# Kernel optimization log

Hardware: AMD Instinct MI355X
Metric: run time of the kernel (lower is better)

Reference implementation:

```python
import jax, jax.numpy as jnp
import numpy as np

B, N, M = 32, 2048, 512
NUM_HEADING_BIN, NUM_SIZE_CLUSTER = 12, 8
OUT_DIM = 3 + 2 * NUM_HEADING_BIN + 4 * NUM_SIZE_CLUSTER  # 59

SPECS = [("sf_w1",64,4),("sf_w2",64,64),("sf_w3",64,64),("sf_w4",128,64),("sf_w5",1024,128),
         ("sh_w1",512,1091),("sh_w2",256,512),("sh_w3",128,256),("sh_w4",128,128),("sh_w5",2,128),
         ("t_w1",128,3),("t_w2",256,128),("t_w3",512,256),("t_fw1",256,515),("t_fw2",128,256),("t_fw3",3,128),
         ("b_w1",128,3),("b_w2",128,128),("b_w3",256,128),("b_w4",512,256),("b_fw1",512,515),("b_fw2",256,512),("b_fw3",OUT_DIM,256)]


def _bn(x, axes):
    # training-mode batch norm, gamma=1 beta=0 (fresh-init torch BatchNorm1d)
    m = jnp.mean(x, axes, keepdims=True)
    v = jnp.var(x, axes, keepdims=True)
    return (x - m) * jax.lax.rsqrt(v + 1e-5)


def _conv(x, w, b):  # 1x1 Conv1d: x (B,C,N), w (O,C), b (O,)
    return jnp.einsum('bcn,oc->bon', x, w) + b[None, :, None]


def _fc(x, w, b):  # x (B,C), w (O,C)
    return x @ w.T + b


def setup_inputs() -> dict:
    key = jax.random.key(0)
    ks = jax.random.split(key, 2 + len(SPECS))
    inp = {}
    inp["point_cloud"] = jax.random.normal(ks[0], (B, N, 4), dtype=jnp.float32)
    cls = jax.random.randint(ks[1], (B,), 0, 3)
    inp["one_hot_vec"] = jax.nn.one_hot(cls, 3, dtype=jnp.float32)
    for i, (nm, o, c) in enumerate(SPECS):
        inp[nm] = jax.random.normal(ks[2 + i], (o, c), dtype=jnp.float32) * (1.0 / np.sqrt(c))
        inp[nm.replace('w', 'b')] = jnp.zeros((o,), jnp.float32)
    return inp


def _forward(point_cloud, one_hot_vec,
             sf_w1, sf_b1, sf_w2, sf_b2, sf_w3, sf_b3, sf_w4, sf_b4, sf_w5, sf_b5,
             sh_w1, sh_b1, sh_w2, sh_b2, sh_w3, sh_b3, sh_w4, sh_b4, sh_w5, sh_b5,
             t_w1, t_b1, t_w2, t_b2, t_w3, t_b3, t_fw1, t_fb1, t_fw2, t_fb2, t_fw3, t_fb3,
             b_w1, b_b1, b_w2, b_b2, b_w3, b_b3, b_w4, b_b4, b_fw1, b_fb1, b_fw2, b_fb2, b_fw3, b_fb3):
    relu = jax.nn.relu
    Bv, Nv = point_cloud.shape[0], point_cloud.shape[1]

    # ---- PointNetSegmentation (PointNetfeat global_feat=False + seg head) ----
    x = point_cloud.transpose(0, 2, 1)                       # (B,4,N)
    h = relu(_bn(_conv(x, sf_w1, sf_b1), (0, 2)))
    pointfeat = relu(_bn(_conv(h, sf_w2, sf_b2), (0, 2)))    # (B,64,N)
    h = relu(_bn(_conv(pointfeat, sf_w3, sf_b3), (0, 2)))
    h = relu(_bn(_conv(h, sf_w4, sf_b4), (0, 2)))
    h = _bn(_conv(h, sf_w5, sf_b5), (0, 2))                  # (B,1024,N), no relu
    g = jnp.max(h, axis=2)                                   # (B,1024)
    g = jnp.concatenate([one_hot_vec, g], axis=1)            # (B,1027)
    feat = jnp.concatenate([jnp.broadcast_to(g[:, :, None], (Bv, 1027, Nv)), pointfeat], axis=1)  # (B,1091,N)
    h = relu(_bn(_conv(feat, sh_w1, sh_b1), (0, 2)))
    h = relu(_bn(_conv(h, sh_w2, sh_b2), (0, 2)))
    h = relu(_bn(_conv(h, sh_w3, sh_b3), (0, 2)))
    h = relu(_bn(_conv(h, sh_w4, sh_b4), (0, 2)))            # dropout p=0.5 -> eval identity
    logits = _conv(h, sh_w5, sh_b5).transpose(0, 2, 1)       # (B,N,2)

    # ---- point_cloud_masking: vectorized mask-select + resample-to-512 ----
    xyz = point_cloud[:, :, :3]
    mask = logits[:, :, 0] < logits[:, :, 1]                 # (B,N) bool
    cnt = jnp.sum(mask, axis=1)                              # (B,)
    mean = jnp.sum(mask[:, :, None] * xyz, axis=1) / jnp.clip(cnt, 1)[:, None].astype(xyz.dtype)
    xyz_c = xyz - mean[:, None, :]                           # centered at mask centroid
    order = jnp.argsort(jnp.logical_not(mask), axis=1, stable=True)  # masked indices first
    u = jax.random.uniform(jax.random.key(42), (Bv, M))
    pos = jnp.minimum((u * cnt[:, None].astype(u.dtype)).astype(jnp.int32),
                      jnp.maximum(cnt[:, None] - 1, 0).astype(jnp.int32))
    idx = jnp.take_along_axis(order, pos, axis=1)            # (B,M) sample w/ replacement from masked set
    object_pc = jnp.take_along_axis(xyz_c, idx[:, :, None], axis=1)  # (B,M,3)
    object_pc = jnp.where(cnt[:, None, None] > 0, object_pc, 0.0)

    x = object_pc.transpose(0, 2, 1)                         # (B,3,M)
    h = relu(_bn(_conv(x, t_w1, t_b1), (0, 2)))
    h = relu(_bn(_conv(h, t_w2, t_b2), (0, 2)))
    h = relu(_bn(_conv(h, t_w3, t_b3), (0, 2)))
    gt = jnp.max(h, axis=2)                                  # (B,512)
    gt = jnp.concatenate([one_hot_vec, gt], axis=1)          # (B,515)
    h = relu(_bn(_fc(gt, t_fw1, t_fb1), 0))
    h = relu(_bn(_fc(h, t_fw2, t_fb2), 0))
    center_delta = _fc(h, t_fw3, t_fb3)                      # (B,3)

    stage1_center = center_delta + mean
    object_pc_new = object_pc - center_delta[:, None, :]

    # ---- PointNet3DboxEstimationNet ----
    x = object_pc_new.transpose(0, 2, 1)                     # (B,3,M)
    h = relu(_bn(_conv(x, b_w1, b_b1), (0, 2)))
    h = relu(_bn(_conv(h, b_w2, b_b2), (0, 2)))
    h = relu(_bn(_conv(h, b_w3, b_b3), (0, 2)))
    h = relu(_bn(_conv(h, b_w4, b_b4), (0, 2)))
    gb = jnp.max(h, axis=2)                                  # (B,512)
    gb = jnp.concatenate([gb, one_hot_vec], axis=1)          # (B,515)
    h = relu(_bn(_fc(gb, b_fw1, b_fb1), 0))
    h = relu(_bn(_fc(h, b_fw2, b_fb2), 0))
    box_out = _fc(h, b_fw3, b_fb3)                           # (B,59)

    center = box_out[:, :3] + stage1_center                  # final box center
    return jnp.concatenate([logits.reshape(Bv, -1), box_out, center], axis=1)  # (B, 2N+59+3)


def reference(point_cloud, one_hot_vec,
              sf_w1, sf_b1, sf_w2, sf_b2, sf_w3, sf_b3, sf_w4, sf_b4, sf_w5, sf_b5,
              sh_w1, sh_b1, sh_w2, sh_b2, sh_w3, sh_b3, sh_w4, sh_b4, sh_w5, sh_b5,
              t_w1, t_b1, t_w2, t_b2, t_w3, t_b3, t_fw1, t_fb1, t_fw2, t_fb2, t_fw3, t_fb3,
              b_w1, b_b1, b_w2, b_b2, b_w3, b_b3, b_w4, b_b4, b_fw1, b_fb1, b_fw2, b_fb2, b_fw3, b_fb3):
    return _forward(point_cloud, one_hot_vec,
                    sf_w1, sf_b1, sf_w2, sf_b2, sf_w3, sf_b3, sf_w4, sf_b4, sf_w5, sf_b5,
                    sh_w1, sh_b1, sh_w2, sh_b2, sh_w3, sh_b3, sh_w4, sh_b4, sh_w5, sh_b5,
                    t_w1, t_b1, t_w2, t_b2, t_w3, t_b3, t_fw1, t_fb1, t_fw2, t_fb2, t_fw3, t_fb3,
                    b_w1, b_b1, b_w2, b_b2, b_w3, b_b3, b_w4, b_b4, b_fw1, b_fb1, b_fw2, b_fb2, b_fw3, b_fb3)
```

## Files before the change

kernel.cpp:

```cpp
#include <hip/hip_runtime.h>
#include <cstdint>


constexpr int PP   = 65536;
constexpr int PP2  = 16384;
constexpr int OUTW = 4158;

constexpr size_t F_Y1 = 0;
constexpr size_t F_Y2 = (size_t)64 * PP;
constexpr size_t F_Y3 = (size_t)128 * PP;
constexpr size_t F_Y4 = (size_t)192 * PP;
constexpr size_t F_P5S = 0;
constexpr size_t F_P5Q = (size_t)2 * 1024 * 1024;
constexpr size_t F_P5M = (size_t)128 * PP;
static_assert(F_P5Q + 2 * 1024 * 1024 <= F_Y2, "P5 partials exceed Y1 slot");
static_assert(F_P5M + 1024 * 1024 <= (size_t)192 * PP, "P5m exceeds Y3 slot");
constexpr size_t F_S1 = (size_t)320 * PP;
constexpr size_t F_S2 = 0;
constexpr size_t F_S3 = (size_t)320 * PP;
constexpr size_t F_S4 = (size_t)448 * PP;
constexpr size_t F_T1 = 0;
constexpr size_t F_T2 = F_T1 + (size_t)128 * PP2;
constexpr size_t F_PT = F_T2 + (size_t)256 * PP2;
constexpr size_t F_B1 = F_PT + (size_t)5 * 256 * 512;
constexpr size_t F_B2 = F_B1 + (size_t)128 * PP2;
constexpr size_t F_B3 = F_B2 + (size_t)128 * PP2;
constexpr size_t F_PB = F_B3 + (size_t)256 * PP2;
static_assert(F_PB + (size_t)5 * 256 * 512 <= (size_t)256 * PP, "t/b overlay overflow");
static_assert((F_PT % 2) == 0 && (F_PB % 2) == 0, "double alignment");

constexpr size_t SB       = (size_t)832 * PP;
constexpr size_t F_MASK   = SB;
constexpr size_t F_MIDX   = F_MASK + PP;
constexpr size_t F_CNT    = F_MIDX + PP;
constexpr size_t F_MEAN   = F_CNT + 32;
constexpr size_t F_GVEC   = F_MEAN + 96;
constexpr size_t F_GVT    = F_GVEC + 32 * 1027;
constexpr size_t F_GVB    = F_GVT + 32 * 515;
constexpr size_t F_GDOT   = F_GVB + 32 * 515;
constexpr size_t F_YT1    = F_GDOT + 512 * 32;
constexpr size_t F_YT2    = F_YT1 + 32 * 256;
constexpr size_t F_YB1    = F_YT2 + 32 * 128;
constexpr size_t F_YB2    = F_YB1 + 32 * 512;
constexpr size_t F_CD     = F_YB2 + 32 * 256;
constexpr size_t F_OBJ    = F_CD + 96;
constexpr size_t F_ST     = F_OBJ + (size_t)3 * PP2;
constexpr size_t F_END    = F_ST + 20 * 2048;
constexpr size_t NEED_BYTES = F_END * 4;

#define NEG_INF (-3.402823466e38f)

__global__ __launch_bounds__(256) void conv_pc_k(const float* __restrict__ pc,
                                                 const float* __restrict__ W,
                                                 const float* __restrict__ bias,
                                                 float* __restrict__ Y) {
  int p = blockIdx.x * 256 + threadIdx.x;
  int o = blockIdx.y;
  float4 v = *reinterpret_cast<const float4*>(&pc[(size_t)p * 4]);
  float s = bias[o] + v.x * W[o * 4 + 0] + v.y * W[o * 4 + 1] + v.z * W[o * 4 + 2] +
            v.w * W[o * 4 + 3];
  Y[(size_t)o * PP + p] = s;
}

__global__ __launch_bounds__(256) void conv_k3_k(const float* __restrict__ Xc,
                                                 const float* __restrict__ W,
                                                 const float* __restrict__ bias,
                                                 const float* __restrict__ cd,
                                                 float* __restrict__ Y) {
  int p = blockIdx.x * 256 + threadIdx.x;
  int o = blockIdx.y;
  int b = p >> 9;
  float x0 = Xc[p], x1 = Xc[PP2 + p], x2 = Xc[2 * PP2 + p];
  if (cd) { x0 -= cd[b * 3]; x1 -= cd[b * 3 + 1]; x2 -= cd[b * 3 + 2]; }
  Y[(size_t)o * PP2 + p] = bias[o] + x0 * W[o * 3] + x1 * W[o * 3 + 1] + x2 * W[o * 3 + 2];
}

template <bool FUSED>
__global__ __launch_bounds__(256) void conv_gemm_k(
    const float* __restrict__ X, int ldx, const float* __restrict__ W, int ldw, int C,
    const float* __restrict__ bias, const float* __restrict__ scale,
    const float* __restrict__ shift, int relu_in, const float* __restrict__ gadd,
    float* __restrict__ Y, int Ptot, double* __restrict__ psum, double* __restrict__ psq,
    float* __restrict__ pmax, int Ototal) {
  __shared__ float Xs[16][64];
  __shared__ float Ws[64][17];
  const int tid = threadIdx.x;
  const int tx = tid & 15, ty = tid >> 4;
  const int o0 = blockIdx.x * 64, p0 = blockIdx.y * 64;
  float acc[4][4] = {};
  for (int c0 = 0; c0 < C; c0 += 16) {
#pragma unroll
    for (int j = 0; j < 4; ++j) {
      int idx = tid + j * 256;
      int k = idx >> 6, n = idx & 63;
      int c = c0 + k;
      float v = 0.f;
      if (c < C) {
        v = X[(size_t)c * ldx + p0 + n];
        if (scale) v = v * scale[c] + shift[c];
        if (relu_in) v = fmaxf(v, 0.f);
      }
      Xs[k][n] = v;
    }
#pragma unroll
    for (int j = 0; j < 4; ++j) {
      int idx = tid + j * 256;
      int o = idx >> 4, k = idx & 15;
      int c = c0 + k;
      Ws[o][k] = (c < C) ? W[(size_t)(o0 + o) * ldw + c] : 0.f;
    }
    __syncthreads();
#pragma unroll
    for (int k = 0; k < 16; ++k) {
      float bx[4], aw[4];
#pragma unroll
      for (int j = 0; j < 4; ++j) bx[j] = Xs[k][tx * 4 + j];
#pragma unroll
      for (int i = 0; i < 4; ++i) aw[i] = Ws[ty * 4 + i][k];
#pragma unroll
      for (int i = 0; i < 4; ++i)
#pragma unroll
        for (int j = 0; j < 4; ++j) acc[i][j] = fmaf(aw[i], bx[j], acc[i][j]);
    }
    __syncthreads();
  }
#pragma unroll
  for (int i = 0; i < 4; ++i) {
    int o = o0 + ty * 4 + i;
    float badd = bias ? bias[o] : 0.f;
    if (gadd) badd += gadd[o * 32 + (p0 >> 11)];
#pragma unroll
    for (int j = 0; j < 4; ++j) acc[i][j] += badd;
  }
  if constexpr (!FUSED) {
#pragma unroll
    for (int i = 0; i < 4; ++i) {
      int o = o0 + ty * 4 + i;
      float4 v = make_float4(acc[i][0], acc[i][1], acc[i][2], acc[i][3]);
      *reinterpret_cast<float4*>(&Y[(size_t)o * Ptot + p0 + tx * 4]) = v;
    }
  } else {
    __shared__ double redd[16][64];
    __shared__ float redf[16][64];
#pragma unroll
    for (int i = 0; i < 4; ++i)
      redd[tx][ty * 4 + i] = (double)acc[i][0] + (double)acc[i][1] +
                             (double)acc[i][2] + (double)acc[i][3];
    __syncthreads();
    if (tid < 64) {
      double s = 0.0;
      for (int t = 0; t < 16; ++t) s += redd[t][tid];
      psum[(size_t)blockIdx.y * Ototal + o0 + tid] = s;
    }
    __syncthreads();
#pragma unroll
    for (int i = 0; i < 4; ++i)
      redd[tx][ty * 4 + i] =
          (double)acc[i][0] * (double)acc[i][0] + (double)acc[i][1] * (double)acc[i][1] +
          (double)acc[i][2] * (double)acc[i][2] + (double)acc[i][3] * (double)acc[i][3];
    __syncthreads();
    if (tid < 64) {
      double s = 0.0;
      for (int t = 0; t < 16; ++t) s += redd[t][tid];
      psq[(size_t)blockIdx.y * Ototal + o0 + tid] = s;
    }
    __syncthreads();
#pragma unroll
    for (int i = 0; i < 4; ++i)
      redf[tx][ty * 4 + i] =
          fmaxf(fmaxf(acc[i][0], acc[i][1]), fmaxf(acc[i][2], acc[i][3]));
    __syncthreads();
    if (tid < 64) {
      float s = NEG_INF;
      for (int t = 0; t < 16; ++t) s = fmaxf(s, redf[t][tid]);
      pmax[(size_t)blockIdx.y * Ototal + o0 + tid] = s;
    }
  }
}

__global__ __launch_bounds__(256) void stats_k(const float* __restrict__ Y, int Ptot,
                                               float* __restrict__ scale,
                                               float* __restrict__ shift) {
  int o = blockIdx.x;
  const float* row = Y + (size_t)o * Ptot;
  double s = 0.0, q = 0.0;
  for (int p = threadIdx.x; p < Ptot; p += 256) {
    double v = (double)row[p];
    s += v;
    q += v * v;
  }
  __shared__ double ss[256], qq[256];
  int tid = threadIdx.x;
  ss[tid] = s; qq[tid] = q;
  __syncthreads();
  for (int off = 128; off; off >>= 1) {
    if (tid < off) { ss[tid] += ss[tid + off]; qq[tid] += qq[tid + off]; }
    __syncthreads();
  }
  if (tid == 0) {
    double m = ss[0] / (double)Ptot;
    double v = qq[0] / (double)Ptot - m * m;
    if (v < 0.0) v = 0.0;
    double sc = 1.0 / sqrt(v + 1e-5);
    scale[o] = (float)sc;
    shift[o] = (float)(-m * sc);
  }
}

__global__ void stats_reduce_k(const double* __restrict__ psum, const double* __restrict__ psq,
                               int ntiles, int O, double invP, float* __restrict__ scale,
                               float* __restrict__ shift) {
  int o = blockIdx.x * blockDim.x + threadIdx.x;
  if (o >= O) return;
  double s = 0.0, q = 0.0;
  for (int t = 0; t < ntiles; ++t) {
    s += psum[(size_t)t * O + o];
    q += psq[(size_t)t * O + o];
  }
  double m = s * invP;
  double v = q * invP - m * m;
  if (v < 0.0) v = 0.0;
  double sc = 1.0 / sqrt(v + 1e-5);
  scale[o] = (float)sc;
  shift[o] = (float)(-m * sc);
}

__global__ void maxpool_g_k(const float* __restrict__ pmax, int tilesPB, int O,
                            const float* __restrict__ scale, const float* __restrict__ shift,
                            int relu, float* __restrict__ out, int ostride, int ooff) {
  int idx = blockIdx.x * blockDim.x + threadIdx.x;
  if (idx >= 32 * O) return;
  int b = idx / O, o = idx - b * O;
  float m = NEG_INF;
  for (int t = b * tilesPB; t < (b + 1) * tilesPB; ++t) m = fmaxf(m, pmax[(size_t)t * O + o]);
  float v = scale[o] * m + shift[o];
  if (relu) v = fmaxf(v, 0.f);
  out[(size_t)b * ostride + ooff + o] = v;
}

__global__ void onehot_k(const float* __restrict__ oh, float* __restrict__ gvec,
                         float* __restrict__ gvt, float* __restrict__ gvb) {
  int i = threadIdx.x;
  if (i >= 96) return;
  int b = i / 3, c = i - b * 3;
  float v = oh[b * 3 + c];
  gvec[b * 1027 + c] = v;
  gvt[b * 515 + c] = v;
  gvb[b * 515 + 512 + c] = v;
}

__global__ void gdot_k(const float* __restrict__ W, const float* __restrict__ gvec,
                       float* __restrict__ gdot) {
  int idx = blockIdx.x * 256 + threadIdx.x;
  int o = idx >> 5, b = idx & 31;
  double s = 0.0;
  const float* wr = W + (size_t)o * 1091;
  const float* gr = gvec + (size_t)b * 1027;
  for (int c = 0; c < 1027; ++c) s += (double)wr[c] * (double)gr[c];
  gdot[o * 32 + b] = (float)s;
}

__global__ __launch_bounds__(256) void logits_k(const float* __restrict__ S4,
                                                const float* __restrict__ W,
                                                const float* __restrict__ bias,
                                                const float* __restrict__ scale,
                                                const float* __restrict__ shift,
                                                float* __restrict__ out,
                                                int* __restrict__ mask) {
  int p = blockIdx.x * 256 + threadIdx.x;
  double l0 = (double)bias[0], l1 = (double)bias[1];
  for (int c = 0; c < 128; ++c) {
    float v = fmaxf(S4[(size_t)c * PP + p] * scale[c] + shift[c], 0.f);
    l0 += (double)v * (double)W[c];
    l1 += (double)v * (double)W[128 + c];
  }
  int b = p >> 11, n = p & 2047;
  out[(size_t)b * OUTW + 2 * n] = (float)l0;
  out[(size_t)b * OUTW + 2 * n + 1] = (float)l1;
  mask[p] = (l0 < l1) ? 1 : 0;
}

__global__ __launch_bounds__(256) void compact_k(const int* __restrict__ mask,
                                                 const float* __restrict__ pc,
                                                 int* __restrict__ midx, int* __restrict__ cnt,
                                                 float* __restrict__ meanv) {
  int b = blockIdx.x, tid = threadIdx.x;
  __shared__ int sc[256];
  __shared__ int base;
  __shared__ double red[256];
  __shared__ double totals[3];
  if (tid == 0) base = 0;
  __syncthreads();
  double sx = 0.0, sy = 0.0, sz = 0.0;
  for (int n0 = 0; n0 < 2048; n0 += 256) {
    int n = n0 + tid;
    int mval = mask[b * 2048 + n];
    sc[tid] = mval;
    __syncthreads();
    for (int off = 1; off < 256; off <<= 1) {
      int v = (tid >= off) ? sc[tid - off] : 0;
      __syncthreads();
      sc[tid] += v;
      __syncthreads();
    }
    int excl = sc[tid] - mval;
    if (mval) {
      midx[b * 2048 + base + excl] = n;
      const float* q = &pc[((size_t)(b * 2048 + n)) * 4];
      sx += (double)q[0]; sy += (double)q[1]; sz += (double)q[2];
    }
    __syncthreads();
    if (tid == 0) base += sc[255];
    __syncthreads();
  }
  red[tid] = sx; __syncthreads();
  for (int off = 128; off; off >>= 1) { if (tid < off) red[tid] += red[tid + off]; __syncthreads(); }
  if (tid == 0) totals[0] = red[0];
  __syncthreads();
  red[tid] = sy; __syncthreads();
  for (int off = 128; off; off >>= 1) { if (tid < off) red[tid] += red[tid + off]; __syncthreads(); }
  if (tid == 0) totals[1] = red[0];
  __syncthreads();
  red[tid] = sz; __syncthreads();
  for (int off = 128; off; off >>= 1) { if (tid < off) red[tid] += red[tid + off]; __syncthreads(); }
  if (tid == 0) {
    totals[2] = red[0];
    int c = base;
    cnt[b] = c;
    double d = (double)(c > 1 ? c : 1);
    meanv[b * 3 + 0] = (float)(totals[0] / d);
    meanv[b * 3 + 1] = (float)(totals[1] / d);
    meanv[b * 3 + 2] = (float)(totals[2] / d);
  }
}

__device__ __forceinline__ uint32_t rotl32(uint32_t x, int r) {
  return (x << r) | (x >> (32 - r));
}
__device__ inline void threefry2x32(uint32_t k0, uint32_t k1, uint32_t& x0, uint32_t& x1) {
  const uint32_t ks[3] = {k0, k1, k0 ^ k1 ^ 0x1BD11BDAu};
  const int rot[2][4] = {{13, 15, 26, 6}, {17, 29, 16, 24}};
  x0 += ks[0]; x1 += ks[1];
  for (int i = 0; i < 5; ++i) {
    const int* r = rot[i & 1];
    for (int j = 0; j < 4; ++j) {
      x0 += x1; x1 = rotl32(x1, r[j]); x1 ^= x0;
    }
    x0 += ks[(i + 1) % 3];
    x1 += ks[(i + 2) % 3] + (uint32_t)(i + 1);
  }
}

__global__ void sample_k(const float* __restrict__ pc, const int* __restrict__ midx,
                         const int* __restrict__ cnt, const float* __restrict__ meanv,
                         float* __restrict__ obj) {
  int e = blockIdx.x * 256 + threadIdx.x;
  if (e >= 16384) return;
  uint32_t x0 = 0u, x1 = (uint32_t)e;
  threefry2x32(0u, 42u, x0, x1);
  uint32_t bits = x0 ^ x1;
  float u = __uint_as_float((bits >> 9) | 0x3F800000u) - 1.0f;
  int b = e >> 9;
  int m = e & 511;
  int c_ = cnt[b];
  int pos = (int)(u * (float)c_);
  int cap = c_ - 1; if (cap < 0) cap = 0;
  if (pos > cap) pos = cap;
  float vx = 0.f, vy = 0.f, vz = 0.f;
  if (c_ > 0) {
    int n = midx[b * 2048 + pos];
    const float* q = &pc[((size_t)(b * 2048 + n)) * 4];
    vx = q[0] - meanv[b * 3 + 0];
    vy = q[1] - meanv[b * 3 + 1];
    vz = q[2] - meanv[b * 3 + 2];
  }
  int p2 = b * 512 + m;
  obj[p2] = vx;
  obj[PP2 + p2] = vy;
  obj[2 * PP2 + p2] = vz;
}

__global__ void fc_gemm_k(const float* __restrict__ Xf, int ldx, int K,
                          const float* __restrict__ W, const float* __restrict__ bias,
                          const float* __restrict__ scale, const float* __restrict__ shift,
                          int relu, float* __restrict__ Y, int ldy, int yoff, int O) {
  int o = blockIdx.x * blockDim.x + threadIdx.x;
  int b = blockIdx.y;
  if (o >= O) return;
  const float* x = Xf + (size_t)b * ldx;
  const float* w = W + (size_t)o * K;
  double s = bias ? (double)bias[o] : 0.0;
  for (int k = 0; k < K; ++k) {
    float v = x[k];
    if (scale) {
      v = v * scale[k] + shift[k];
      if (relu) v = fmaxf(v, 0.f);
    }
    s += (double)v * (double)w[k];
  }
  Y[(size_t)b * ldy + yoff + o] = (float)s;
}

__global__ void fc_stats_k(const float* __restrict__ Y, int ldy, int O,
                           float* __restrict__ scale, float* __restrict__ shift) {
  int o = blockIdx.x * blockDim.x + threadIdx.x;
  if (o >= O) return;
  double s = 0.0, q = 0.0;
  for (int b = 0; b < 32; ++b) {
    double v = (double)Y[(size_t)b * ldy + o];
    s += v;
    q += v * v;
  }
  double m = s / 32.0;
  double v = q / 32.0 - m * m;
  if (v < 0.0) v = 0.0;
  double sc = 1.0 / sqrt(v + 1e-5);
  scale[o] = (float)sc;
  shift[o] = (float)(-m * sc);
}

__global__ void center_k(float* __restrict__ out, const float* __restrict__ cd,
                         const float* __restrict__ meanv) {
  int i = threadIdx.x;
  if (i >= 96) return;
  int b = i / 3, c = i - b * 3;
  out[(size_t)b * OUTW + 4155 + c] =
      out[(size_t)b * OUTW + 4096 + c] + cd[b * 3 + c] + meanv[b * 3 + c];
}

__global__ void size_fail_k(float* out, float code) {
  if (threadIdx.x == 0 && blockIdx.x == 0) out[0] = code;
}

extern "C" void kernel_launch(void* const* d_in, const int* in_sizes, int n_in, void* d_out,
                              int out_size, void* d_ws, size_t ws_size, hipStream_t stream) {
  float* out = (float*)d_out;
  static const int EXP[48] = {
      262144, 96, 256, 64, 4096, 64, 4096, 64, 8192, 128, 131072, 1024,
      558592, 512, 131072, 256, 32768, 128, 16384, 128, 256, 2,
      384, 128, 32768, 256, 131072, 512, 131840, 256, 32768, 128, 384, 3,
      384, 128, 16384, 128, 32768, 256, 131072, 512, 263680, 512, 131072, 256,
      15104, 59};
  if (n_in != 48) { size_fail_k<<<1, 1, 0, stream>>>(out, 9.0e6f + 99.0f * 1e4f); return; }
  if (out_size != 133056) { size_fail_k<<<1, 1, 0, stream>>>(out, 9.0e6f + 98.0f * 1e4f); return; }
  for (int i = 0; i < 48; ++i)
    if (in_sizes[i] != EXP[i]) {
      size_fail_k<<<1, 1, 0, stream>>>(out, 9.0e6f + (float)i * 1e4f);
      return;
    }
  if (ws_size < NEED_BYTES) { size_fail_k<<<1, 1, 0, stream>>>(out, 9.0e6f + 97.0f * 1e4f); return; }

  const float* pc = (const float*)d_in[0];
  const float* oh = (const float*)d_in[1];
#define IN(i) ((const float*)d_in[i])
  float* ws = (float*)d_ws;
  auto SC = [&](int s) { return ws + F_ST + (size_t)s * 2048; };
  auto SH = [&](int s) { return ws + F_ST + (size_t)s * 2048 + 1024; };
  enum { L_C1, L_C2, L_C3, L_C4, L_C5, L_S1, L_S2, L_S3, L_S4, L_T1, L_T2, L_T3,
         L_B1, L_B2, L_B3, L_B4, L_FT1, L_FT2, L_FB1, L_FB2 };

  float* Y1 = ws + F_Y1;
  float* Y2 = ws + F_Y2;
  float* Y3 = ws + F_Y3;
  float* Y4 = ws + F_Y4;
  double* P5s = (double*)(ws + F_P5S);
  double* P5q = (double*)(ws + F_P5Q);
  float*  P5m = ws + F_P5M;
  float* S1 = ws + F_S1;
  float* S2 = ws + F_S2;
  float* S3 = ws + F_S3;
  float* S4 = ws + F_S4;
  int* mask = (int*)(ws + F_MASK);
  int* midx = (int*)(ws + F_MIDX);
  int* cnt = (int*)(ws + F_CNT);
  float* meanv = ws + F_MEAN;
  float* gvec = ws + F_GVEC;
  float* gvt = ws + F_GVT;
  float* gvb = ws + F_GVB;
  float* gdot = ws + F_GDOT;
  float* obj = ws + F_OBJ;
  float* T1 = ws + F_T1;
  float* T2 = ws + F_T2;
  float* Bb1 = ws + F_B1;
  float* Bb2 = ws + F_B2;
  float* Bb3 = ws + F_B3;
  double* PTs = (double*)(ws + F_PT);
  double* PTq = (double*)(ws + F_PT + (size_t)2 * 256 * 512);
  float*  PTm = ws + F_PT + (size_t)4 * 256 * 512;
  double* PBs = (double*)(ws + F_PB);
  double* PBq = (double*)(ws + F_PB + (size_t)2 * 256 * 512);
  float*  PBm = ws + F_PB + (size_t)4 * 256 * 512;
  float* yt1 = ws + F_YT1;
  float* yt2 = ws + F_YT2;
  float* yb1 = ws + F_YB1;
  float* yb2 = ws + F_YB2;
  float* cd = ws + F_CD;

  dim3 blk(256);
  conv_pc_k<<<dim3(PP / 256, 64), blk, 0, stream>>>(pc, IN(2), IN(3), Y1);
  stats_k<<<64, blk, 0, stream>>>(Y1, PP, SC(L_C1), SH(L_C1));
  conv_gemm_k<false><<<dim3(1, PP / 64), blk, 0, stream>>>(Y1, PP, IN(4), 64, 64, IN(5),
      SC(L_C1), SH(L_C1), 1, nullptr, Y2, PP, nullptr, nullptr, nullptr, 0);
  stats_k<<<64, blk, 0, stream>>>(Y2, PP, SC(L_C2), SH(L_C2));
  conv_gemm_k<false><<<dim3(1, PP / 64), blk, 0, stream>>>(Y2, PP, IN(6), 64, 64, IN(7),
      SC(L_C2), SH(L_C2), 1, nullptr, Y3, PP, nullptr, nullptr, nullptr, 0);
  stats_k<<<64, blk, 0, stream>>>(Y3, PP, SC(L_C3), SH(L_C3));
  conv_gemm_k<false><<<dim3(2, PP / 64), blk, 0, stream>>>(Y3, PP, IN(8), 64, 64, IN(9),
      SC(L_C3), SH(L_C3), 1, nullptr, Y4, PP, nullptr, nullptr, nullptr, 0);
  stats_k<<<128, blk, 0, stream>>>(Y4, PP, SC(L_C4), SH(L_C4));
  conv_gemm_k<true><<<dim3(16, PP / 64), blk, 0, stream>>>(Y4, PP, IN(10), 128, 128, IN(11),
      SC(L_C4), SH(L_C4), 1, nullptr, nullptr, PP, P5s, P5q, P5m, 1024);
  stats_reduce_k<<<4, blk, 0, stream>>>(P5s, P5q, 1024, 1024, 1.0 / PP, SC(L_C5), SH(L_C5));
  onehot_k<<<1, 96, 0, stream>>>(oh, gvec, gvt, gvb);
  maxpool_g_k<<<(32 * 1024) / 256, blk, 0, stream>>>(P5m, 32, 1024, SC(L_C5), SH(L_C5), 0,
                                                     gvec, 1027, 3);
  gdot_k<<<64, blk, 0, stream>>>(IN(12), gvec, gdot);
  conv_gemm_k<false><<<dim3(8, PP / 64), blk, 0, stream>>>(Y2, PP, IN(12) + 1027, 1091, 64,
      IN(13), SC(L_C2), SH(L_C2), 1, gdot, S1, PP, nullptr, nullptr, nullptr, 0);
  stats_k<<<512, blk, 0, stream>>>(S1, PP, SC(L_S1), SH(L_S1));
  conv_gemm_k<false><<<dim3(4, PP / 64), blk, 0, stream>>>(S1, PP, IN(14), 512, 512, IN(15),
      SC(L_S1), SH(L_S1), 1, nullptr, S2, PP, nullptr, nullptr, nullptr, 0);
  stats_k<<<256, blk, 0, stream>>>(S2, PP, SC(L_S2), SH(L_S2));
  conv_gemm_k<false><<<dim3(2, PP / 64), blk, 0, stream>>>(S2, PP, IN(16), 256, 256, IN(17),
      SC(L_S2), SH(L_S2), 1, nullptr, S3, PP, nullptr, nullptr, nullptr, 0);
  stats_k<<<128, blk, 0, stream>>>(S3, PP, SC(L_S3), SH(L_S3));
  conv_gemm_k<false><<<dim3(2, PP / 64), blk, 0, stream>>>(S3, PP, IN(18), 128, 128, IN(19),
      SC(L_S3), SH(L_S3), 1, nullptr, S4, PP, nullptr, nullptr, nullptr, 0);
  stats_k<<<128, blk, 0, stream>>>(S4, PP, SC(L_S4), SH(L_S4));
  logits_k<<<PP / 256, blk, 0, stream>>>(S4, IN(20), IN(21), SC(L_S4), SH(L_S4), out, mask);
  compact_k<<<32, blk, 0, stream>>>(mask, pc, midx, cnt, meanv);
  sample_k<<<64, blk, 0, stream>>>(pc, midx, cnt, meanv, obj);
  conv_k3_k<<<dim3(PP2 / 256, 128), blk, 0, stream>>>(obj, IN(22), IN(23), nullptr, T1);
  stats_k<<<128, blk, 0, stream>>>(T1, PP2, SC(L_T1), SH(L_T1));
  conv_gemm_k<false><<<dim3(4, PP2 / 64), blk, 0, stream>>>(T1, PP2, IN(24), 128, 128, IN(25),
      SC(L_T1), SH(L_T1), 1, nullptr, T2, PP2, nullptr, nullptr, nullptr, 0);
  stats_k<<<256, blk, 0, stream>>>(T2, PP2, SC(L_T2), SH(L_T2));
  conv_gemm_k<true><<<dim3(8, PP2 / 64), blk, 0, stream>>>(T2, PP2, IN(26), 256, 256, IN(27),
      SC(L_T2), SH(L_T2), 1, nullptr, nullptr, PP2, PTs, PTq, PTm, 512);
  stats_reduce_k<<<2, blk, 0, stream>>>(PTs, PTq, 256, 512, 1.0 / PP2, SC(L_T3), SH(L_T3));
  maxpool_g_k<<<(32 * 512) / 256, blk, 0, stream>>>(PTm, 8, 512, SC(L_T3), SH(L_T3), 1, gvt,
                                                    515, 3);
  fc_gemm_k<<<dim3(1, 32), blk, 0, stream>>>(gvt, 515, 515, IN(28), IN(29), nullptr, nullptr,
                                             0, yt1, 256, 0, 256);
  fc_stats_k<<<1, blk, 0, stream>>>(yt1, 256, 256, SC(L_FT1), SH(L_FT1));
  fc_gemm_k<<<dim3(1, 32), blk, 0, stream>>>(yt1, 256, 256, IN(30), IN(31), SC(L_FT1),
                                             SH(L_FT1), 1, yt2, 128, 0, 128);
  fc_stats_k<<<1, blk, 0, stream>>>(yt2, 128, 128, SC(L_FT2), SH(L_FT2));
  fc_gemm_k<<<dim3(1, 32), blk, 0, stream>>>(yt2, 128, 128, IN(32), IN(33), SC(L_FT2),
                                             SH(L_FT2), 1, cd, 3, 0, 3);
  conv_k3_k<<<dim3(PP2 / 256, 128), blk, 0, stream>>>(obj, IN(34), IN(35), cd, Bb1);
  stats_k<<<128, blk, 0, stream>>>(Bb1, PP2, SC(L_B1), SH(L_B1));
  conv_gemm_k<false><<<dim3(2, PP2 / 64), blk, 0, stream>>>(Bb1, PP2, IN(36), 128, 128, IN(37),
      SC(L_B1), SH(L_B1), 1, nullptr, Bb2, PP2, nullptr, nullptr, nullptr, 0);
  stats_k<<<128, blk, 0, stream>>>(Bb2, PP2, SC(L_B2), SH(L_B2));
  conv_gemm_k<false><<<dim3(4, PP2 / 64), blk, 0, stream>>>(Bb2, PP2, IN(38), 128, 128, IN(39),
      SC(L_B2), SH(L_B2), 1, nullptr, Bb3, PP2, nullptr, nullptr, nullptr, 0);
  stats_k<<<256, blk, 0, stream>>>(Bb3, PP2, SC(L_B3), SH(L_B3));
  conv_gemm_k<true><<<dim3(8, PP2 / 64), blk, 0, stream>>>(Bb3, PP2, IN(40), 256, 256, IN(41),
      SC(L_B3), SH(L_B3), 1, nullptr, nullptr, PP2, PBs, PBq, PBm, 512);
  stats_reduce_k<<<2, blk, 0, stream>>>(PBs, PBq, 256, 512, 1.0 / PP2, SC(L_B4), SH(L_B4));
  maxpool_g_k<<<(32 * 512) / 256, blk, 0, stream>>>(PBm, 8, 512, SC(L_B4), SH(L_B4), 1, gvb,
                                                    515, 0);
  fc_gemm_k<<<dim3(2, 32), blk, 0, stream>>>(gvb, 515, 515, IN(42), IN(43), nullptr, nullptr,
                                             0, yb1, 512, 0, 512);
  fc_stats_k<<<2, blk, 0, stream>>>(yb1, 512, 512, SC(L_FB1), SH(L_FB1));
  fc_gemm_k<<<dim3(1, 32), blk, 0, stream>>>(yb1, 512, 512, IN(44), IN(45), SC(L_FB1),
                                             SH(L_FB1), 1, yb2, 256, 0, 256);
  fc_stats_k<<<1, blk, 0, stream>>>(yb2, 256, 256, SC(L_FB2), SH(L_FB2));
  fc_gemm_k<<<dim3(1, 32), blk, 0, stream>>>(yb2, 256, 256, IN(46), IN(47), SC(L_FB2),
                                             SH(L_FB2), 1, out, OUTW, 4096, 59);
  center_k<<<1, 96, 0, stream>>>(out, cd, meanv);
#undef IN
}
```

Measured before the change: 2.987 ms.

## Add 128x128 register-tiled GEMM kernel for larger pointwise convolutions

Introduces gemm_big_k, which uses 128x128 output tiles with 8x8 per-thread accumulators, float4 shared-memory loads and a transposed weight tile. It is used for every pointwise conv with at least 64 output channels past the first two layers, and the partial-reduction counts passed to stats_reduce and maxpool are updated for the new tile size. The aim is more arithmetic per shared-memory load and fewer global re-reads of activations, at the cost of higher register pressure and fewer blocks. The small kernel also drops its channel bounds checks, which assumes C is a multiple of 16.

After: 2.417 ms. -19.1%, faster.

```diff
diff --git a/kernel.cpp b/kernel.cpp
--- a/kernel.cpp
+++ b/kernel.cpp
@@ -75,13 +75,10 @@
   Y[(size_t)o * PP2 + p] = bias[o] + x0 * W[o * 3] + x1 * W[o * 3 + 1] + x2 * W[o * 3 + 2];
 }
 
-template <bool FUSED>
 __global__ __launch_bounds__(256) void conv_gemm_k(
     const float* __restrict__ X, int ldx, const float* __restrict__ W, int ldw, int C,
     const float* __restrict__ bias, const float* __restrict__ scale,
-    const float* __restrict__ shift, int relu_in, const float* __restrict__ gadd,
-    float* __restrict__ Y, int Ptot, double* __restrict__ psum, double* __restrict__ psq,
-    float* __restrict__ pmax, int Ototal) {
+    const float* __restrict__ shift, int relu_in, float* __restrict__ Y, int Ptot) {
   __shared__ float Xs[16][64];
   __shared__ float Ws[64][17];
   const int tid = threadIdx.x;
@@ -94,20 +91,16 @@
       int idx = tid + j * 256;
       int k = idx >> 6, n = idx & 63;
       int c = c0 + k;
-      float v = 0.f;
-      if (c < C) {
-        v = X[(size_t)c * ldx + p0 + n];
-        if (scale) v = v * scale[c] + shift[c];
-        if (relu_in) v = fmaxf(v, 0.f);
-      }
+      float v = X[(size_t)c * ldx + p0 + n];
+      if (scale) v = v * scale[c] + shift[c];
+      if (relu_in) v = fmaxf(v, 0.f);
       Xs[k][n] = v;
     }
 #pragma unroll
     for (int j = 0; j < 4; ++j) {
       int idx = tid + j * 256;
       int o = idx >> 4, k = idx & 15;
-      int c = c0 + k;
-      Ws[o][k] = (c < C) ? W[(size_t)(o0 + o) * ldw + c] : 0.f;
+      Ws[o][k] = W[(size_t)(o0 + o) * ldw + c0 + k];
     }
     __syncthreads();
 #pragma unroll
@@ -127,53 +120,130 @@
 #pragma unroll
   for (int i = 0; i < 4; ++i) {
     int o = o0 + ty * 4 + i;
+    float badd = bias[o];
+#pragma unroll
+    for (int j = 0; j < 4; ++j) acc[i][j] += badd;
+  }
+#pragma unroll
+  for (int i = 0; i < 4; ++i) {
+    int o = o0 + ty * 4 + i;
+    float4 v = make_float4(acc[i][0], acc[i][1], acc[i][2], acc[i][3]);
+    *reinterpret_cast<float4*>(&Y[(size_t)o * Ptot + p0 + tx * 4]) = v;
+  }
+}
+
+template <bool FUSED>
+__global__ __launch_bounds__(256) void gemm_big_k(
+    const float* __restrict__ X, int ldx, const float* __restrict__ W, int ldw, int C,
+    const float* __restrict__ bias, const float* __restrict__ scale,
+    const float* __restrict__ shift, int relu_in, const float* __restrict__ gadd,
+    float* __restrict__ Y, int Ptot, double* __restrict__ psum, double* __restrict__ psq,
+    float* __restrict__ pmax, int Ototal) {
+  __shared__ float Xs[16][128];
+  __shared__ float Wt[16][128];
+  const int tid = threadIdx.x;
+  const int tx = tid & 15, ty = tid >> 4;
+  const int o0 = blockIdx.x * 128, p0 = blockIdx.y * 128;
+  float acc[8][8] = {};
+  for (int c0 = 0; c0 < C; c0 += 16) {
+#pragma unroll
+    for (int q = 0; q < 2; ++q) {
+      int f = tid + q * 256;
+      int k = f >> 5, c4 = f & 31;
+      int c = c0 + k;
+      float4 v = *reinterpret_cast<const float4*>(&X[(size_t)c * ldx + p0 + c4 * 4]);
+      if (scale) {
+        float sc = scale[c], sh = shift[c];
+        v.x = v.x * sc + sh; v.y = v.y * sc + sh;
+        v.z = v.z * sc + sh; v.w = v.w * sc + sh;
+      }
+      if (relu_in) {
+        v.x = fmaxf(v.x, 0.f); v.y = fmaxf(v.y, 0.f);
+        v.z = fmaxf(v.z, 0.f); v.w = fmaxf(v.w, 0.f);
+      }
+      *reinterpret_cast<float4*>(&Xs[k][c4 * 4]) = v;
+    }
+#pragma unroll
+    for (int q = 0; q < 8; ++q) {
+      int idx = tid + q * 256;
+      int k = idx >> 7, o = idx & 127;
+      Wt[k][o] = W[(size_t)(o0 + o) * ldw + c0 + k];
+    }
+    __syncthreads();
+#pragma unroll
+    for (int k = 0; k < 16; ++k) {
+      float bx[8], aw[8];
+      *reinterpret_cast<float4*>(&bx[0]) = *reinterpret_cast<const float4*>(&Xs[k][tx * 8]);
+      *reinterpret_cast<float4*>(&bx[4]) = *reinterpret_cast<const float4*>(&Xs[k][tx * 8 + 4]);
+      *reinterpret_cast<float4*>(&aw[0]) = *reinterpret_cast<const float4*>(&Wt[k][ty * 8]);
+      *reinterpret_cast<float4*>(&aw[4]) = *reinterpret_cast<const float4*>(&Wt[k][ty * 8 + 4]);
+#pragma unroll
+      for (int i = 0; i < 8; ++i)
+#pragma unroll
+        for (int j = 0; j < 8; ++j) acc[i][j] = fmaf(aw[i], bx[j], acc[i][j]);
+    }
+    __syncthreads();
+  }
+#pragma unroll
+  for (int i = 0; i < 8; ++i) {
+    int o = o0 + ty * 8 + i;
     float badd = bias ? bias[o] : 0.f;
     if (gadd) badd += gadd[o * 32 + (p0 >> 11)];
 #pragma unroll
-    for (int j = 0; j < 4; ++j) acc[i][j] += badd;
+    for (int j = 0; j < 8; ++j) acc[i][j] += badd;
   }
   if constexpr (!FUSED) {
 #pragma unroll
-    for (int i = 0; i < 4; ++i) {
-      int o = o0 + ty * 4 + i;
-      float4 v = make_float4(acc[i][0], acc[i][1], acc[i][2], acc[i][3]);
-      *reinterpret_cast<float4*>(&Y[(size_t)o * Ptot + p0 + tx * 4]) = v;
+    for (int i = 0; i < 8; ++i) {
+      int o = o0 + ty * 8 + i;
+      float* dst = &Y[(size_t)o * Ptot + p0 + tx * 8];
+      *reinterpret_cast<float4*>(dst) =
+          make_float4(acc[i][0], acc[i][1], acc[i][2], acc[i][3]);
+      *reinterpret_cast<float4*>(dst + 4) =
+          make_float4(acc[i][4], acc[i][5], acc[i][6], acc[i][7]);
     }
   } else {
-    __shared__ double redd[16][64];
-    __shared__ float redf[16][64];
-#pragma unroll
-    for (int i = 0; i < 4; ++i)
-      redd[tx][ty * 4 + i] = (double)acc[i][0] + (double)acc[i][1] +
-                             (double)acc[i][2] + (double)acc[i][3];
-    __syncthreads();
-    if (tid < 64) {
+    __shared__ double redd[16][128];
+#pragma unroll
+    for (int i = 0; i < 8; ++i) {
+      double s = 0.0;
+#pragma unroll
+      for (int j = 0; j < 8; ++j) s += (double)acc[i][j];
+      redd[tx][ty * 8 + i] = s;
+    }
+    __syncthreads();
+    if (tid < 128) {
       double s = 0.0;
       for (int t = 0; t < 16; ++t) s += redd[t][tid];
       psum[(size_t)blockIdx.y * Ototal + o0 + tid] = s;
     }
     __syncthreads();
 #pragma unroll
-    for (int i = 0; i < 4; ++i)
-      redd[tx][ty * 4 + i] =
-          (double)acc[i][0] * (double)acc[i][0] + (double)acc[i][1] * (double)acc[i][1] +
-          (double)acc[i][2] * (double)acc[i][2] + (double)acc[i][3] * (double)acc[i][3];
-    __syncthreads();
-    if (tid < 64) {
+    for (int i = 0; i < 8; ++i) {
+      double s = 0.0;
+#pragma unroll
+      for (int j = 0; j < 8; ++j) s += (double)acc[i][j] * (double)acc[i][j];
+      redd[tx][ty * 8 + i] = s;
+    }
+    __syncthreads();
+    if (tid < 128) {
       double s = 0.0;
       for (int t = 0; t < 16; ++t) s += redd[t][tid];
       psq[(size_t)blockIdx.y * Ototal + o0 + tid] = s;
     }
     __syncthreads();
 #pragma unroll
-    for (int i = 0; i < 4; ++i)
-      redf[tx][ty * 4 + i] =
-          fmaxf(fmaxf(acc[i][0], acc[i][1]), fmaxf(acc[i][2], acc[i][3]));
-    __syncthreads();
-    if (tid < 64) {
-      float s = NEG_INF;
-      for (int t = 0; t < 16; ++t) s = fmaxf(s, redf[t][tid]);
-      pmax[(size_t)blockIdx.y * Ototal + o0 + tid] = s;
+    for (int i = 0; i < 8; ++i) {
+      float mx = acc[i][0];
+#pragma unroll
+      for (int j = 1; j < 8; ++j) mx = fmaxf(mx, acc[i][j]);
+      redd[tx][ty * 8 + i] = (double)mx;
+    }
+    __syncthreads();
+    if (tid < 128) {
+      double s = -1.0e300;
+      for (int t = 0; t < 16; ++t) s = s > redd[t][tid] ? s : redd[t][tid];
+      pmax[(size_t)blockIdx.y * Ototal + o0 + tid] = (float)s;
     }
   }
 }
@@ -499,32 +569,33 @@
   dim3 blk(256);
   conv_pc_k<<<dim3(PP / 256, 64), blk, 0, stream>>>(pc, IN(2), IN(3), Y1);
   stats_k<<<64, blk, 0, stream>>>(Y1, PP, SC(L_C1), SH(L_C1));
-  conv_gemm_k<false><<<dim3(1, PP / 64), blk, 0, stream>>>(Y1, PP, IN(4), 64, 64, IN(5),
-      SC(L_C1), SH(L_C1), 1, nullptr, Y2, PP, nullptr, nullptr, nullptr, 0);
+  conv_gemm_k<<<dim3(1, PP / 64), blk, 0, stream>>>(Y1, PP, IN(4), 64, 64, IN(5),
+      SC(L_C1), SH(L_C1), 1, Y2, PP);
   stats_k<<<64, blk, 0, stream>>>(Y2, PP, SC(L_C2), SH(L_C2));
-  conv_gemm_k<false><<<dim3(1, PP / 64), blk, 0, stream>>>(Y2, PP, IN(6), 64, 64, IN(7),
-      SC(L_C2), SH(L_C2), 1, nullptr, Y3, PP, nullptr, nullptr, nullptr, 0);
+  conv_gemm_k<<<dim3(1, PP / 64), blk, 0, stream>>>(Y2, PP, IN(6), 64, 64, IN(7),
+      SC(L_C2), SH(L_C2), 1, Y3, PP);
   stats_k<<<64, blk, 0, stream>>>(Y3, PP, SC(L_C3), SH(L_C3));
-  conv_gemm_k<false><<<dim3(2, PP / 64), blk, 0, stream>>>(Y3, PP, IN(8), 64, 64, IN(9),
+  gemm_big_k<false><<<dim3(1, PP / 128), blk, 0, stream>>>(Y3, PP, IN(8), 64, 64, IN(9),
       SC(L_C3), SH(L_C3), 1, nullptr, Y4, PP, nullptr, nullptr, nullptr, 0);
   stats_k<<<128, blk, 0, stream>>>(Y4, PP, SC(L_C4), SH(L_C4));
-  conv_gemm_k<true><<<dim3(16, PP / 64), blk, 0, stream>>>(Y4, PP, IN(10), 128, 128, IN(11),
+  gemm_big_k<true><<<dim3(8, PP / 128), blk, 0, stream>>>(Y4, PP, IN(10), 128, 128, IN(11),
       SC(L_C4), SH(L_C4), 1, nullptr, nullptr, PP, P5s, P5q, P5m, 1024);
-  stats_reduce_k<<<4, blk, 0, stream>>>(P5s, P5q, 1024, 1024, 1.0 / PP, SC(L_C5), SH(L_C5));
+  stats_reduce_k<<<4, blk, 0, stream>>>(P5s, P5q, PP / 128, 1024, 1.0 / PP, SC(L_C5),
+                                        SH(L_C5));
   onehot_k<<<1, 96, 0, stream>>>(oh, gvec, gvt, gvb);
-  maxpool_g_k<<<(32 * 1024) / 256, blk, 0, stream>>>(P5m, 32, 1024, SC(L_C5), SH(L_C5), 0,
+  maxpool_g_k<<<(32 * 1024) / 256, blk, 0, stream>>>(P5m, 16, 1024, SC(L_C5), SH(L_C5), 0,
                                                      gvec, 1027, 3);
   gdot_k<<<64, blk, 0, stream>>>(IN(12), gvec, gdot);
-  conv_gemm_k<false><<<dim3(8, PP / 64), blk, 0, stream>>>(Y2, PP, IN(12) + 1027, 1091, 64,
+  gemm_big_k<false><<<dim3(4, PP / 128), blk, 0, stream>>>(Y2, PP, IN(12) + 1027, 1091, 64,
       IN(13), SC(L_C2), SH(L_C2), 1, gdot, S1, PP, nullptr, nullptr, nullptr, 0);
   stats_k<<<512, blk, 0, stream>>>(S1, PP, SC(L_S1), SH(L_S1));
-  conv_gemm_k<false><<<dim3(4, PP / 64), blk, 0, stream>>>(S1, PP, IN(14), 512, 512, IN(15),
+  gemm_big_k<false><<<dim3(2, PP / 128), blk, 0, stream>>>(S1, PP, IN(14), 512, 512, IN(15),
       SC(L_S1), SH(L_S1), 1, nullptr, S2, PP, nullptr, nullptr, nullptr, 0);
   stats_k<<<256, blk, 0, stream>>>(S2, PP, SC(L_S2), SH(L_S2));
-  conv_gemm_k<false><<<dim3(2, PP / 64), blk, 0, stream>>>(S2, PP, IN(16), 256, 256, IN(17),
+  gemm_big_k<false><<<dim3(1, PP / 128), blk, 0, stream>>>(S2, PP, IN(16), 256, 256, IN(17),
       SC(L_S2), SH(L_S2), 1, nullptr, S3, PP, nullptr, nullptr, nullptr, 0);
   stats_k<<<128, blk, 0, stream>>>(S3, PP, SC(L_S3), SH(L_S3));
-  conv_gemm_k<false><<<dim3(2, PP / 64), blk, 0, stream>>>(S3, PP, IN(18), 128, 128, IN(19),
+  gemm_big_k<false><<<dim3(1, PP / 128), blk, 0, stream>>>(S3, PP, IN(18), 128, 128, IN(19),
       SC(L_S3), SH(L_S3), 1, nullptr, S4, PP, nullptr, nullptr, nullptr, 0);
   stats_k<<<128, blk, 0, stream>>>(S4, PP, SC(L_S4), SH(L_S4));
   logits_k<<<PP / 256, blk, 0, stream>>>(S4, IN(20), IN(21), SC(L_S4), SH(L_S4), out, mask);
@@ -532,13 +603,14 @@
   sample_k<<<64, blk, 0, stream>>>(pc, midx, cnt, meanv, obj);
   conv_k3_k<<<dim3(PP2 / 256, 128), blk, 0, stream>>>(obj, IN(22), IN(23), nullptr, T1);
   stats_k<<<128, blk, 0, stream>>>(T1, PP2, SC(L_T1), SH(L_T1));
-  conv_gemm_k<false><<<dim3(4, PP2 / 64), blk, 0, stream>>>(T1, PP2, IN(24), 128, 128, IN(25),
-      SC(L_T1), SH(L_T1), 1, nullptr, T2, PP2, nullptr, nullptr, nullptr, 0);
+  gemm_big_k<false><<<dim3(2, PP2 / 128), blk, 0, stream>>>(T1, PP2, IN(24), 128, 128,
+      IN(25), SC(L_T1), SH(L_T1), 1, nullptr, T2, PP2, nullptr, nullptr, nullptr, 0);
   stats_k<<<256, blk, 0, stream>>>(T2, PP2, SC(L_T2), SH(L_T2));
-  conv_gemm_k<true><<<dim3(8, PP2 / 64), blk, 0, stream>>>(T2, PP2, IN(26), 256, 256, IN(27),
-      SC(L_T2), SH(L_T2), 1, nullptr, nullptr, PP2, PTs, PTq, PTm, 512);
-  stats_reduce_k<<<2, blk, 0, stream>>>(PTs, PTq, 256, 512, 1.0 / PP2, SC(L_T3), SH(L_T3));
-  maxpool_g_k<<<(32 * 512) / 256, blk, 0, stream>>>(PTm, 8, 512, SC(L_T3), SH(L_T3), 1, gvt,
+  gemm_big_k<true><<<dim3(4, PP2 / 128), blk, 0, stream>>>(T2, PP2, IN(26), 256, 256,
+      IN(27), SC(L_T2), SH(L_T2), 1, nullptr, nullptr, PP2, PTs, PTq, PTm, 512);
+  stats_reduce_k<<<2, blk, 0, stream>>>(PTs, PTq, PP2 / 128, 512, 1.0 / PP2, SC(L_T3),
+                                        SH(L_T3));
+  maxpool_g_k<<<(32 * 512) / 256, blk, 0, stream>>>(PTm, 4, 512, SC(L_T3), SH(L_T3), 1, gvt,
                                                     515, 3);
   fc_gemm_k<<<dim3(1, 32), blk, 0, stream>>>(gvt, 515, 515, IN(28), IN(29), nullptr, nullptr,
                                              0, yt1, 256, 0, 256);
@@ -550,16 +622,17 @@
                                              SH(L_FT2), 1, cd, 3, 0, 3);
   conv_k3_k<<<dim3(PP2 / 256, 128), blk, 0, stream>>>(obj, IN(34), IN(35), cd, Bb1);
   stats_k<<<128, blk, 0, stream>>>(Bb1, PP2, SC(L_B1), SH(L_B1));
-  conv_gemm_k<false><<<dim3(2, PP2 / 64), blk, 0, stream>>>(Bb1, PP2, IN(36), 128, 128, IN(37),
-      SC(L_B1), SH(L_B1), 1, nullptr, Bb2, PP2, nullptr, nullptr, nullptr, 0);
+  gemm_big_k<false><<<dim3(1, PP2 / 128), blk, 0, stream>>>(Bb1, PP2, IN(36), 128, 128,
+      IN(37), SC(L_B1), SH(L_B1), 1, nullptr, Bb2, PP2, nullptr, nullptr, nullptr, 0);
   stats_k<<<128, blk, 0, stream>>>(Bb2, PP2, SC(L_B2), SH(L_B2));
-  conv_gemm_k<false><<<dim3(4, PP2 / 64), blk, 0, stream>>>(Bb2, PP2, IN(38), 128, 128, IN(39),
-      SC(L_B2), SH(L_B2), 1, nullptr, Bb3, PP2, nullptr, nullptr, nullptr, 0);
+  gemm_big_k<false><<<dim3(2, PP2 / 128), blk, 0, stream>>>(Bb2, PP2, IN(38), 128, 128,
+      IN(39), SC(L_B2), SH(L_B2), 1, nullptr, Bb3, PP2, nullptr, nullptr, nullptr, 0);
   stats_k<<<256, blk, 0, stream>>>(Bb3, PP2, SC(L_B3), SH(L_B3));
-  conv_gemm_k<true><<<dim3(8, PP2 / 64), blk, 0, stream>>>(Bb3, PP2, IN(40), 256, 256, IN(41),
-      SC(L_B3), SH(L_B3), 1, nullptr, nullptr, PP2, PBs, PBq, PBm, 512);
-  stats_reduce_k<<<2, blk, 0, stream>>>(PBs, PBq, 256, 512, 1.0 / PP2, SC(L_B4), SH(L_B4));
-  maxpool_g_k<<<(32 * 512) / 256, blk, 0, stream>>>(PBm, 8, 512, SC(L_B4), SH(L_B4), 1, gvb,
+  gemm_big_k<true><<<dim3(4, PP2 / 128), blk, 0, stream>>>(Bb3, PP2, IN(40), 256, 256,
+      IN(41), SC(L_B3), SH(L_B3), 1, nullptr, nullptr, PP2, PBs, PBq, PBm, 512);
+  stats_reduce_k<<<2, blk, 0, stream>>>(PBs, PBq, PP2 / 128, 512, 1.0 / PP2, SC(L_B4),
+                                        SH(L_B4));
+  maxpool_g_k<<<(32 * 512) / 256, blk, 0, stream>>>(PBm, 4, 512, SC(L_B4), SH(L_B4), 1, gvb,
                                                     515, 0);
   fc_gemm_k<<<dim3(2, 32), blk, 0, stream>>>(gvb, 515, 515, IN(42), IN(43), nullptr, nullptr,
                                              0, yb1, 512, 0, 512);
```
